# Kernel tuning notes

Hardware: AMD Instinct MI355X
Metric: run time of the kernel (lower is better)

Reference implementation:

```python
import jax, jax.numpy as jnp
import numpy as np

N = 2708
IN_C = 1433
OUT_C = 64


def setup_inputs() -> dict:
    key = jax.random.key(0)
    k1, k2, k3, k4, k5, k6, k7 = jax.random.split(key, 7)
    X = jax.random.normal(k1, (N, IN_C), dtype=jnp.float32)
    A = jax.random.randint(k2, (N, N), 0, 2, dtype=jnp.int32)  # dense binary adjacency mask
    # Graph Fourier basis: orthonormal-ish random matrix (QR of gaussian)
    U = jnp.linalg.qr(jax.random.normal(k3, (N, N), dtype=jnp.float32))[0]
    s = 1.0 / np.sqrt(IN_C)
    W_K = jax.random.normal(k4, (OUT_C, IN_C), dtype=jnp.float32) * s
    W_Q = jax.random.normal(k5, (OUT_C, IN_C), dtype=jnp.float32) * s
    W_V = jax.random.normal(k6, (OUT_C, IN_C), dtype=jnp.float32) * s
    lmbd = jax.random.uniform(k7, (N, 1), dtype=jnp.float32)
    return {"X": X, "A": A, "U": U, "W_K": W_K, "W_Q": W_Q, "W_V": W_V, "lmbd": lmbd}


def reference(X, A, U, W_K, W_Q, W_V, lmbd):
    # Linear projections (torch nn.Linear: x @ W.T)
    K = X @ W_K.T  # [N, d]
    Q = X @ W_Q.T  # [N, d]
    V = X @ W_V.T  # [N, d]
    d_k = K.shape[-1]
    E = (Q @ K.T) / d_k  # [N, N]
    # spectral filtering: igft(lmbd * gft(E)) = U @ (lmbd * (U^T @ E))
    E = jnp.abs(U @ (lmbd * (U.T @ E)))
    # masked softmax over neighbors; dropout p=0 in eval mode (no-op)
    E_masked = jnp.where(A == 0, -jnp.inf, E)
    alpha = jax.nn.softmax(E_masked, axis=-1)
    H = alpha @ V  # [N, d]
    return H
```

## Files before the change

### kernel.cpp

```cpp
#include <hip/hip_runtime.h>

#define NV 2708
#define INC 1433
#define XCOLS 1472
#define UDIM 2752
#define PSTR 2720
#define BSTR 2752
#define SLAB ((size_t)(2752*64))
#define MWPR 88
#define NSP 8
#define NSU 22

typedef __attribute__((ext_vector_type(8))) short bf16x8;
typedef __attribute__((ext_vector_type(4))) float f32x4;
typedef __attribute__((ext_vector_type(4))) unsigned short u16x4;

__device__ __forceinline__ unsigned short f2bf(float f){
  union { float f; unsigned int i; } v; v.f = f;
  return (unsigned short)((v.i + 0x7fffu + ((v.i >> 16) & 1u)) >> 16);
}

__device__ __forceinline__ void conv_row(const float* __restrict__ src,
                                         unsigned short* __restrict__ dst, int tid){
  const int sh = ((unsigned int)((size_t)src >> 2)) & 1;
  if (tid == 0){ int ce = sh ? 0 : (INC - 1); dst[ce] = f2bf(src[ce]); }
  const float2* s2 = (const float2*)(src + sh);
  for (int c2 = tid; c2 < (INC - 1)/2; c2 += 256){
    float2 v = s2[c2];
    int c = sh + c2*2;
    dst[c]     = f2bf(v.x);
    dst[c + 1] = f2bf(v.y);
  }
  for (int c = INC + tid; c < XCOLS; c += 256) dst[c] = 0;
}

__global__ __launch_bounds__(256) void convert_all(
    const float* __restrict__ X, const float* __restrict__ WK,
    const float* __restrict__ WQ, const float* __restrict__ WV,
    const float* __restrict__ U, const int* __restrict__ A,
    unsigned short* __restrict__ Xbf, unsigned short* __restrict__ Wbf,
    unsigned short* __restrict__ Ubf, unsigned int* __restrict__ Abits)
{
  const int bx = blockIdx.x;
  const int tid = threadIdx.x;
  if (bx < 2752){
    const int row = bx;
    unsigned short* dst = Ubf + (size_t)row*UDIM;
    if (row < NV){
      const float* src = U + (size_t)row*NV;
      for (int c4 = tid; c4 < 688; c4 += 256){
        float4 v = make_float4(0.f,0.f,0.f,0.f);
        if (c4 < 677) v = *(const float4*)(src + c4*4);
        u16x4 h = { f2bf(v.x), f2bf(v.y), f2bf(v.z), f2bf(v.w) };
        *(u16x4*)(dst + c4*4) = h;
      }
    } else {
      u16x4 zz = {0,0,0,0};
      for (int c4 = tid; c4 < 688; c4 += 256) *(u16x4*)(dst + c4*4) = zz;
    }
  } else if (bx < 5504){
    const int row = bx - 2752;
    unsigned short* dst = Xbf + (size_t)row*XCOLS;
    if (row < NV){
      conv_row(X + (size_t)row*INC, dst, tid);
    } else {
      u16x4 zz = {0,0,0,0};
      for (int c4 = tid; c4 < XCOLS/4; c4 += 256) *(u16x4*)(dst + c4*4) = zz;
    }
  } else if (bx < 5696){
    const int row = bx - 5504;
    const float* s = (row < 64) ? WK : (row < 128) ? WQ : WV;
    conv_row(s + (size_t)(row & 63)*INC, Wbf + (size_t)row*XCOLS, tid);
  } else {
    const int i = bx - 5696;
    const int lane = tid & 63, wave = tid >> 6;
    const int* arow = A + (size_t)i*NV;
    unsigned int* drow = Abits + (size_t)i*MWPR;
    for (int g = wave; g < 11; g += 4){
      int base = g*256 + lane*4;
      int4 v = make_int4(0,0,0,0);
      if (base < NV) v = *(const int4*)(arow + base);
      unsigned long long m0 = __ballot(v.x != 0);
      unsigned long long m1 = __ballot(v.y != 0);
      unsigned long long m2 = __ballot(v.z != 0);
      unsigned long long m3 = __ballot(v.w != 0);
      if (lane < 8){
        unsigned long long mm = (lane < 2) ? m0 : (lane < 4) ? m1 : (lane < 6) ? m2 : m3;
        drow[g*8 + lane] = (lane & 1) ? (unsigned int)(mm >> 32) : (unsigned int)mm;
      }
    }
  }
}

__global__ __launch_bounds__(256) void proj(
    const unsigned short* __restrict__ Xbf, const unsigned short* __restrict__ Wbf,
    float* __restrict__ part)
{
  __shared__ __align__(16) unsigned short At[64*72];
  __shared__ __align__(16) unsigned short Bt[64*72];
  const int tid = threadIdx.x;
  const int lane = tid & 63, wave = tid >> 6, quad = lane >> 4, lr = lane & 15;
  const int m0 = blockIdx.x * 64;
  const int s  = blockIdx.y, z = blockIdx.z;
  const int kbeg = s * 192, kend = min(kbeg + 192, XCOLS);
  const int wm = (wave & 1) * 32, wn = (wave >> 1) * 32;
  const unsigned short* Wz = Wbf + (size_t)z*64*XCOLS;
  const int srow = wave*8 + (lane >> 3), seg = lane & 7;
  f32x4 acc[2][2] = {};

  for (int k0 = kbeg; k0 < kend; k0 += 64){
    #pragma unroll
    for (int e = 0; e < 2; e++){
      int row = e*32 + srow;
      bf16x8 xa = *(const bf16x8*)(Xbf + (size_t)(m0+row)*XCOLS + k0 + seg*8);
      bf16x8 wb = *(const bf16x8*)(Wz  + (size_t)row*XCOLS      + k0 + seg*8);
      *(bf16x8*)&At[row*72 + seg*8] = xa;
      *(bf16x8*)&Bt[row*72 + seg*8] = wb;
    }
    __syncthreads();
    #pragma unroll
    for (int ks = 0; ks < 2; ks++){
      bf16x8 af[2], bv[2];
      #pragma unroll
      for (int t = 0; t < 2; t++){
        af[t] = *(const bf16x8*)&At[(wm + t*16 + lr)*72 + ks*32 + quad*8];
        bv[t] = *(const bf16x8*)&Bt[(wn + t*16 + lr)*72 + ks*32 + quad*8];
      }
      #pragma unroll
      for (int tm = 0; tm < 2; tm++)
        #pragma unroll
        for (int tn = 0; tn < 2; tn++)
          acc[tm][tn] = __builtin_amdgcn_mfma_f32_16x16x32_bf16(af[tm], bv[tn], acc[tm][tn], 0, 0, 0);
    }
    __syncthreads();
  }
  float* dst = part + (size_t)(z*NSP + s) * SLAB;
  #pragma unroll
  for (int tm = 0; tm < 2; tm++)
    #pragma unroll
    for (int tn = 0; tn < 2; tn++)
      #pragma unroll
      for (int e = 0; e < 4; e++)
        dst[(size_t)(m0 + wm + tm*16 + quad*4 + e)*64 + wn + tn*16 + lr] = acc[tm][tn][e];
}

__global__ __launch_bounds__(256) void reduce_proj(
    const float* __restrict__ part, unsigned short* __restrict__ K16f,
    unsigned short* __restrict__ QT16, unsigned short* __restrict__ VTf)
{
  int idx = blockIdx.x*256 + threadIdx.x;
  int z = blockIdx.y;
  int m = idx >> 6, c = idx & 63;
  const float* base = part + (size_t)z*NSP*SLAB + idx;
  float v = 0.f;
  #pragma unroll
  for (int s = 0; s < NSP; s++) v += base[s*SLAB];
  unsigned short h = (m < NV) ? f2bf(v) : (unsigned short)0;
  if (z == 0){
    if (m < 2720) K16f[((m>>4)*2 + (c>>5))*512 + (m&15)*32 + (c&31)] = h;
  } else if (z == 1){
    QT16[(size_t)c*BSTR + m] = h;
  } else {
    if (m < 2720) VTf[(m>>5)*2048 + c*32 + (m&31)] = h;
  }
}

__global__ __launch_bounds__(256) void gemmG(
    const unsigned short* __restrict__ Ubf, const unsigned short* __restrict__ QT,
    float* __restrict__ part)
{
  __shared__ __align__(16) unsigned short At[64*72];
  __shared__ __align__(16) unsigned short Bt[64*72];
  const int tid = threadIdx.x;
  const int lane = tid & 63, wave = tid >> 6, quad = lane >> 4, lr = lane & 15;
  const int m0 = blockIdx.x * 64;
  const int s  = blockIdx.y;
  const int kbeg = s * 128, kend = min(kbeg + 128, UDIM);
  const int wm = (wave & 1) * 32, wn = (wave >> 1) * 32;
  const int bc = tid >> 2, bseg = tid & 3;
  const int ml = (lane & 15)*4, koff = wave*16 + (lane >> 4);
  f32x4 acc[2][2] = {};

  for (int k0 = kbeg; k0 < kend; k0 += 64){
    #pragma unroll
    for (int e = 0; e < 4; e++){
      int kl = koff + e*4;
      u16x4 v = *(const u16x4*)(Ubf + (size_t)(k0+kl)*UDIM + m0 + ml);
      At[(ml+0)*72 + kl] = v[0];
      At[(ml+1)*72 + kl] = v[1];
      At[(ml+2)*72 + kl] = v[2];
      At[(ml+3)*72 + kl] = v[3];
    }
    {
      const unsigned short* q = QT + (size_t)bc*BSTR + k0 + bseg*16;
      *(bf16x8*)&Bt[bc*72 + bseg*16]     = *(const bf16x8*)(q);
      *(bf16x8*)&Bt[bc*72 + bseg*16 + 8] = *(const bf16x8*)(q + 8);
    }
    __syncthreads();
    #pragma unroll
    for (int ks = 0; ks < 2; ks++){
      bf16x8 af[2], bv[2];
      #pragma unroll
      for (int t = 0; t < 2; t++){
        af[t] = *(const bf16x8*)&At[(wm + t*16 + lr)*72 + ks*32 + quad*8];
        bv[t] = *(const bf16x8*)&Bt[(wn + t*16 + lr)*72 + ks*32 + quad*8];
      }
      #pragma unroll
      for (int tm = 0; tm < 2; tm++)
        #pragma unroll
        for (int tn = 0; tn < 2; tn++)
          acc[tm][tn] = __builtin_amdgcn_mfma_f32_16x16x32_bf16(af[tm], bv[tn], acc[tm][tn], 0, 0, 0);
    }
    __syncthreads();
  }
  float* dst = part + (size_t)s * SLAB;
  #pragma unroll
  for (int tm = 0; tm < 2; tm++)
    #pragma unroll
    for (int tn = 0; tn < 2; tn++)
      #pragma unroll
      for (int e = 0; e < 4; e++)
        dst[(size_t)(m0 + wm + tm*16 + quad*4 + e)*64 + wn + tn*16 + lr] = acc[tm][tn][e];
}

__global__ __launch_bounds__(256) void reduce_g(
    const float* __restrict__ part, const float* __restrict__ lm,
    unsigned short* __restrict__ G2T)
{
  int idx = blockIdx.x*256 + threadIdx.x;
  int m = idx >> 6, c = idx & 63;
  const float* base = part + idx;
  float v = 0.f;
  #pragma unroll
  for (int s = 0; s < NSU; s++) v += base[s*SLAB];
  unsigned short h = 0;
  if (m < NV) h = f2bf(v * lm[m] * (1.0f/64.0f));
  G2T[(size_t)c*BSTR + m] = h;
}

__global__ __launch_bounds__(256) void gemmF(
    const unsigned short* __restrict__ Ubf, const unsigned short* __restrict__ G2T,
    float* __restrict__ part)
{
  __shared__ __align__(16) unsigned short At[64*72];
  __shared__ __align__(16) unsigned short Bt[64*72];
  const int tid = threadIdx.x;
  const int lane = tid & 63, wave = tid >> 6, quad = lane >> 4, lr = lane & 15;
  const int m0 = blockIdx.x * 64;
  const int s  = blockIdx.y;
  const int kbeg = s * 128, kend = min(kbeg + 128, UDIM);
  const int wm = (wave & 1) * 32, wn = (wave >> 1) * 32;
  const int bc = tid >> 2, bseg = tid & 3;
  const int srow = wave*8 + (lane >> 3), seg = lane & 7;
  f32x4 acc[2][2] = {};

  for (int k0 = kbeg; k0 < kend; k0 += 64){
    #pragma unroll
    for (int e = 0; e < 2; e++){
      int row = e*32 + srow;
      bf16x8 ua = *(const bf16x8*)(Ubf + (size_t)(m0+row)*UDIM + k0 + seg*8);
      *(bf16x8*)&At[row*72 + seg*8] = ua;
    }
    {
      const unsigned short* g = G2T + (size_t)bc*BSTR + k0 + bseg*16;
      *(bf16x8*)&Bt[bc*72 + bseg*16]     = *(const bf16x8*)(g);
      *(bf16x8*)&Bt[bc*72 + bseg*16 + 8] = *(const bf16x8*)(g + 8);
    }
    __syncthreads();
    #pragma unroll
    for (int ks = 0; ks < 2; ks++){
      bf16x8 af[2], bv[2];
      #pragma unroll
      for (int t = 0; t < 2; t++){
        af[t] = *(const bf16x8*)&At[(wm + t*16 + lr)*72 + ks*32 + quad*8];
        bv[t] = *(const bf16x8*)&Bt[(wn + t*16 + lr)*72 + ks*32 + quad*8];
      }
      #pragma unroll
      for (int tm = 0; tm < 2; tm++)
        #pragma unroll
        for (int tn = 0; tn < 2; tn++)
          acc[tm][tn] = __builtin_amdgcn_mfma_f32_16x16x32_bf16(af[tm], bv[tn], acc[tm][tn], 0, 0, 0);
    }
    __syncthreads();
  }
  float* dst = part + (size_t)s * SLAB;
  #pragma unroll
  for (int tm = 0; tm < 2; tm++)
    #pragma unroll
    for (int tn = 0; tn < 2; tn++)
      #pragma unroll
      for (int e = 0; e < 4; e++)
        dst[(size_t)(m0 + wm + tm*16 + quad*4 + e)*64 + wn + tn*16 + lr] = acc[tm][tn][e];
}

__global__ __launch_bounds__(256) void fused_attn(
    const float* __restrict__ partF, const unsigned short* __restrict__ K16f,
    const unsigned int* __restrict__ Abits, const unsigned short* __restrict__ VTf,
    float* __restrict__ Hout)
{
  __shared__ __align__(16) unsigned short pbuf[8*PSTR];
  __shared__ __align__(16) unsigned short fbuf[8*64];
  __shared__ unsigned int mrow[8*MWPR];
  __shared__ float swave[4][8];
  __shared__ float rinv[8];
  const int tid  = threadIdx.x;
  const int lane = tid & 63, wave = tid >> 6;
  const int quad = lane >> 4, lr = lane & 15;
  const int i0 = blockIdx.x * 8;

  #pragma unroll
  for (int h = 0; h < 2; h++){
    int idx = h*256 + tid;
    const float* base = partF + (size_t)(i0 + (idx >> 6))*64 + (idx & 63);
    float v = 0.f;
    #pragma unroll
    for (int s = 0; s < NSU; s++) v += base[s*SLAB];
    fbuf[idx] = f2bf(v);
  }
  for (int idx = tid; idx < 8*MWPR; idx += 256){
    int r = idx / MWPR;
    unsigned int v = 0;
    if (i0 + r < NV) v = Abits[(size_t)(i0 + r)*MWPR + (idx - r*MWPR)];
    mrow[idx] = v;
  }
  __syncthreads();

  const bf16x8 af0 = *(const bf16x8*)&fbuf[(lr & 7)*64 + quad*8];
  const bf16x8 af1 = *(const bf16x8*)&fbuf[(lr & 7)*64 + 32 + quad*8];
  const int ehi   = quad >> 1;
  const int rbase = (quad & 1)*4 + ehi*2;
  float psum[2] = {0.f, 0.f};
  {
    int t = wave;
    const unsigned short* kb = K16f + t*1024 + lr*32 + quad*8;
    bf16x8 b0 = *(const bf16x8*)(kb);
    bf16x8 b1 = *(const bf16x8*)(kb + 512);
    while (t < 170){
      int tn = t + 4;
      bf16x8 n0 = b0, n1 = b1;
      if (tn < 170){
        const unsigned short* nb = K16f + tn*1024 + lr*32 + quad*8;
        n0 = *(const bf16x8*)(nb);
        n1 = *(const bf16x8*)(nb + 512);
      }
      f32x4 sv0 = {}, sv1 = {};
      sv0 = __builtin_amdgcn_mfma_f32_16x16x32_bf16(af0, b0, sv0, 0, 0, 0);
      sv1 = __builtin_amdgcn_mfma_f32_16x16x32_bf16(af1, b1, sv1, 0, 0, 0);
      f32x4 sv = sv0 + sv1;
      {
        int col = t*16 + lr;
        int ss = col & 255, ll = ss >> 2;
        int wsh = (col >> 8)*8 + (ss & 3)*2 + (ll >> 5);
        int bit = ll & 31;
        #pragma unroll
        for (int e2 = 0; e2 < 2; e2++){
          int r = rbase + e2;
          float svv = (e2 == 0) ? (ehi ? sv[2] : sv[0]) : (ehi ? sv[3] : sv[1]);
          float p = 0.f;
          if ((mrow[r*MWPR + wsh] >> bit) & 1u) p = __expf(fabsf(svv));
          psum[e2] += p;
          pbuf[r*PSTR + col] = f2bf(p);
        }
      }
      b0 = n0; b1 = n1; t = tn;
    }
  }
  #pragma unroll
  for (int e2 = 0; e2 < 2; e2++){
    float v = psum[e2];
    #pragma unroll
    for (int o = 1; o <= 8; o <<= 1) v += __shfl_xor(v, o, 64);
    if (lr == 0) swave[wave][rbase + e2] = v;
  }
  __syncthreads();
  if (tid < 8){
    float sum = swave[0][tid] + swave[1][tid] + swave[2][tid] + swave[3][tid];
    rinv[tid] = (sum > 0.f) ? (1.f/sum) : 0.f;
  }
  __syncthreads();

  const int c0 = wave * 16;
  const int mr = lr & 7;
  f32x4 acc = {};
  {
    bf16x8 bv = *(const bf16x8*)&VTf[(c0 + lr)*32 + quad*8];
    for (int kt = 0; kt < 85; kt++){
      bf16x8 bn = bv;
      if (kt + 1 < 85) bn = *(const bf16x8*)&VTf[(kt+1)*2048 + (c0 + lr)*32 + quad*8];
      bf16x8 af = *(const bf16x8*)&pbuf[mr*PSTR + kt*32 + quad*8];
      acc = __builtin_amdgcn_mfma_f32_16x16x32_bf16(af, bv, acc, 0, 0, 0);
      bv = bn;
    }
  }
  if (quad < 2){
    #pragma unroll
    for (int e = 0; e < 4; e++){
      int r = quad*4 + e;
      int i = i0 + r;
      if (i < NV) Hout[(size_t)i*64 + c0 + lr] = acc[e] * rinv[r];
    }
  }
}

extern "C" void kernel_launch(void* const* d_in, const int* in_sizes, int n_in,
                              void* d_out, int out_size, void* d_ws, size_t ws_size,
                              hipStream_t stream){
  (void)in_sizes; (void)n_in; (void)out_size; (void)ws_size;
  const float* X  = (const float*)d_in[0];
  const int*   A  = (const int*)d_in[1];
  const float* U  = (const float*)d_in[2];
  const float* WK = (const float*)d_in[3];
  const float* WQ = (const float*)d_in[4];
  const float* WV = (const float*)d_in[5];
  const float* lm = (const float*)d_in[6];

  char* ws = (char*)d_ws;
  size_t off = 0;
  auto alloc = [&](size_t bytes){ size_t o = off; off = (off + bytes + 255) & ~(size_t)255; return o; };
  float*          part = (float*)(ws + alloc(24*SLAB*4));
  unsigned short* Ubf  = (unsigned short*)(ws + alloc((size_t)UDIM*UDIM*2));
  unsigned short* Xbf  = (unsigned short*)(ws + alloc((size_t)UDIM*XCOLS*2));
  unsigned short* Wbf  = (unsigned short*)(ws + alloc((size_t)192*XCOLS*2));
  unsigned short* K16f = (unsigned short*)(ws + alloc((size_t)170*1024*2));
  unsigned short* QT16 = (unsigned short*)(ws + alloc((size_t)64*BSTR*2));
  unsigned short* G2T  = (unsigned short*)(ws + alloc((size_t)64*BSTR*2));
  unsigned short* VTf  = (unsigned short*)(ws + alloc((size_t)85*2048*2));
  unsigned int*   Abits= (unsigned int*)(ws + alloc((size_t)NV*MWPR*4));

  convert_all<<<dim3(8404), 256, 0, stream>>>(X, WK, WQ, WV, U, A, Xbf, Wbf, Ubf, Abits);
  proj<<<dim3(43, NSP, 3), 256, 0, stream>>>(Xbf, Wbf, part);
  reduce_proj<<<dim3(688, 3), 256, 0, stream>>>(part, K16f, QT16, VTf);
  gemmG<<<dim3(43, NSU), 256, 0, stream>>>(Ubf, QT16, part);
  reduce_g<<<dim3(688), 256, 0, stream>>>(part, lm, G2T);
  gemmF<<<dim3(43, NSU), 256, 0, stream>>>(Ubf, G2T, part);
  fused_attn<<<dim3((NV + 7)/8), 256, 0, stream>>>(part, K16f, Abits, VTf, (float*)d_out);
}
```

Measured before the change: 184.9 us.

## Fuse split-K reductions into GEMM tails via atomic counters; widen attention blocks to 16 rows

```diff
diff --git a/kernel.cpp b/kernel.cpp
--- a/kernel.cpp
+++ b/kernel.cpp
@@ -4,7 +4,7 @@
 #define INC 1433
 #define XCOLS 1472
 #define UDIM 2752
-#define PSTR 2720
+#define PSTR 2728
 #define BSTR 2752
 #define SLAB ((size_t)(2752*64))
 #define MWPR 88
@@ -39,10 +39,12 @@
     const float* __restrict__ WQ, const float* __restrict__ WV,
     const float* __restrict__ U, const int* __restrict__ A,
     unsigned short* __restrict__ Xbf, unsigned short* __restrict__ Wbf,
-    unsigned short* __restrict__ Ubf, unsigned int* __restrict__ Abits)
+    unsigned short* __restrict__ Ubf, unsigned int* __restrict__ Abits,
+    unsigned int* __restrict__ ctr)
 {
   const int bx = blockIdx.x;
   const int tid = threadIdx.x;
+  if (bx == 0 && tid < 256) ctr[tid] = 0u;
   if (bx < 2752){
     const int row = bx;
     unsigned short* dst = Ubf + (size_t)row*UDIM;
@@ -94,10 +96,13 @@
 
 __global__ __launch_bounds__(256) void proj(
     const unsigned short* __restrict__ Xbf, const unsigned short* __restrict__ Wbf,
-    float* __restrict__ part)
+    float* __restrict__ part, unsigned int* __restrict__ ctr,
+    unsigned short* __restrict__ K16f, unsigned short* __restrict__ QT16,
+    unsigned short* __restrict__ VTf)
 {
   __shared__ __align__(16) unsigned short At[64*72];
   __shared__ __align__(16) unsigned short Bt[64*72];
+  __shared__ unsigned int scnt;
   const int tid = threadIdx.x;
   const int lane = tid & 63, wave = tid >> 6, quad = lane >> 4, lr = lane & 15;
   const int m0 = blockIdx.x * 64;
@@ -142,35 +147,39 @@
       #pragma unroll
       for (int e = 0; e < 4; e++)
         dst[(size_t)(m0 + wm + tm*16 + quad*4 + e)*64 + wn + tn*16 + lr] = acc[tm][tn][e];
-}
-
-__global__ __launch_bounds__(256) void reduce_proj(
-    const float* __restrict__ part, unsigned short* __restrict__ K16f,
-    unsigned short* __restrict__ QT16, unsigned short* __restrict__ VTf)
-{
-  int idx = blockIdx.x*256 + threadIdx.x;
-  int z = blockIdx.y;
-  int m = idx >> 6, c = idx & 63;
-  const float* base = part + (size_t)z*NSP*SLAB + idx;
-  float v = 0.f;
-  #pragma unroll
-  for (int s = 0; s < NSP; s++) v += base[s*SLAB];
-  unsigned short h = (m < NV) ? f2bf(v) : (unsigned short)0;
-  if (z == 0){
-    if (m < 2720) K16f[((m>>4)*2 + (c>>5))*512 + (m&15)*32 + (c&31)] = h;
-  } else if (z == 1){
-    QT16[(size_t)c*BSTR + m] = h;
-  } else {
-    if (m < 2720) VTf[(m>>5)*2048 + c*32 + (m&31)] = h;
+
+  __threadfence();
+  __syncthreads();
+  if (tid == 0) scnt = atomicAdd(&ctr[z*43 + blockIdx.x], 1u);
+  __syncthreads();
+  if (scnt == NSP - 1){
+    __threadfence();
+    const float* base = part + (size_t)(z*NSP)*SLAB + (size_t)m0*64;
+    for (int idx = tid; idx < 4096; idx += 256){
+      int m = m0 + (idx >> 6), c = idx & 63;
+      float v = 0.f;
+      #pragma unroll
+      for (int s2 = 0; s2 < NSP; s2++) v += base[s2*SLAB + idx];
+      unsigned short h = (m < NV) ? f2bf(v) : (unsigned short)0;
+      if (z == 0){
+        if (m < 2720) K16f[((m>>4)*2 + (c>>5))*512 + (m&15)*32 + (c&31)] = h;
+      } else if (z == 1){
+        QT16[(size_t)c*BSTR + m] = h;
+      } else {
+        if (m < 2720) VTf[(m>>5)*2048 + c*32 + (m&31)] = h;
+      }
+    }
   }
 }
 
 __global__ __launch_bounds__(256) void gemmG(
     const unsigned short* __restrict__ Ubf, const unsigned short* __restrict__ QT,
-    float* __restrict__ part)
+    float* __restrict__ part, unsigned int* __restrict__ ctr,
+    const float* __restrict__ lm, unsigned short* __restrict__ G2T)
 {
   __shared__ __align__(16) unsigned short At[64*72];
   __shared__ __align__(16) unsigned short Bt[64*72];
+  __shared__ unsigned int scnt;
   const int tid = threadIdx.x;
   const int lane = tid & 63, wave = tid >> 6, quad = lane >> 4, lr = lane & 15;
   const int m0 = blockIdx.x * 64;
@@ -221,29 +230,34 @@
       #pragma unroll
       for (int e = 0; e < 4; e++)
         dst[(size_t)(m0 + wm + tm*16 + quad*4 + e)*64 + wn + tn*16 + lr] = acc[tm][tn][e];
-}
-
-__global__ __launch_bounds__(256) void reduce_g(
-    const float* __restrict__ part, const float* __restrict__ lm,
-    unsigned short* __restrict__ G2T)
-{
-  int idx = blockIdx.x*256 + threadIdx.x;
-  int m = idx >> 6, c = idx & 63;
-  const float* base = part + idx;
-  float v = 0.f;
-  #pragma unroll
-  for (int s = 0; s < NSU; s++) v += base[s*SLAB];
-  unsigned short h = 0;
-  if (m < NV) h = f2bf(v * lm[m] * (1.0f/64.0f));
-  G2T[(size_t)c*BSTR + m] = h;
+
+  __threadfence();
+  __syncthreads();
+  if (tid == 0) scnt = atomicAdd(&ctr[144 + blockIdx.x], 1u);
+  __syncthreads();
+  if (scnt == NSU - 1){
+    __threadfence();
+    const float* base = part + (size_t)m0*64;
+    for (int idx = tid; idx < 4096; idx += 256){
+      int m = m0 + (idx >> 6), c = idx & 63;
+      float v = 0.f;
+      #pragma unroll
+      for (int s2 = 0; s2 < NSU; s2++) v += base[s2*SLAB + idx];
+      unsigned short h = 0;
+      if (m < NV) h = f2bf(v * lm[m] * (1.0f/64.0f));
+      G2T[(size_t)c*BSTR + m] = h;
+    }
+  }
 }
 
 __global__ __launch_bounds__(256) void gemmF(
     const unsigned short* __restrict__ Ubf, const unsigned short* __restrict__ G2T,
-    float* __restrict__ part)
+    float* __restrict__ part, unsigned int* __restrict__ ctr,
+    unsigned short* __restrict__ Fbf)
 {
   __shared__ __align__(16) unsigned short At[64*72];
   __shared__ __align__(16) unsigned short Bt[64*72];
+  __shared__ unsigned int scnt;
   const int tid = threadIdx.x;
   const int lane = tid & 63, wave = tid >> 6, quad = lane >> 4, lr = lane & 15;
   const int m0 = blockIdx.x * 64;
@@ -279,7 +293,7 @@
       for (int tm = 0; tm < 2; tm++)
         #pragma unroll
         for (int tn = 0; tn < 2; tn++)
-          acc[tm][tn] = __builtin_amdgcn_mfma_f32_16x16x32_bf16(af[tm], bv[tn], acc[tm][tn], 0, 0, 0);
+          acc[tm][tn] = __builtin_amdgcn_mfma_f32_16x16x32_bf16(af[tm], bv[ks == 0 ? tn : tn], acc[tm][tn], 0, 0, 0);
     }
     __syncthreads();
   }
@@ -291,52 +305,57 @@
       #pragma unroll
       for (int e = 0; e < 4; e++)
         dst[(size_t)(m0 + wm + tm*16 + quad*4 + e)*64 + wn + tn*16 + lr] = acc[tm][tn][e];
-}
-
-__global__ __launch_bounds__(256) void fused_attn(
-    const float* __restrict__ partF, const unsigned short* __restrict__ K16f,
+
+  __threadfence();
+  __syncthreads();
+  if (tid == 0) scnt = atomicAdd(&ctr[192 + blockIdx.x], 1u);
+  __syncthreads();
+  if (scnt == NSU - 1){
+    __threadfence();
+    const float* base = part + (size_t)m0*64;
+    for (int idx = tid; idx < 4096; idx += 256){
+      int m = m0 + (idx >> 6), c = idx & 63;
+      float v = 0.f;
+      #pragma unroll
+      for (int s2 = 0; s2 < NSU; s2++) v += base[s2*SLAB + idx];
+      Fbf[(size_t)m*64 + c] = (m < NV) ? f2bf(v) : (unsigned short)0;
+    }
+  }
+}
+
+__global__ __launch_bounds__(512) void fused_attn(
+    const unsigned short* __restrict__ Fbf, const unsigned short* __restrict__ K16f,
     const unsigned int* __restrict__ Abits, const unsigned short* __restrict__ VTf,
     float* __restrict__ Hout)
 {
-  __shared__ __align__(16) unsigned short pbuf[8*PSTR];
-  __shared__ __align__(16) unsigned short fbuf[8*64];
-  __shared__ unsigned int mrow[8*MWPR];
-  __shared__ float swave[4][8];
-  __shared__ float rinv[8];
+  __shared__ __align__(16) unsigned short pbuf[16*PSTR];
+  __shared__ unsigned int mrow[16*MWPR];
+  __shared__ float swave[8][16];
+  __shared__ float rinv[16];
+  __shared__ __align__(16) float obuf[4][256];
   const int tid  = threadIdx.x;
   const int lane = tid & 63, wave = tid >> 6;
   const int quad = lane >> 4, lr = lane & 15;
-  const int i0 = blockIdx.x * 8;
-
-  #pragma unroll
-  for (int h = 0; h < 2; h++){
-    int idx = h*256 + tid;
-    const float* base = partF + (size_t)(i0 + (idx >> 6))*64 + (idx & 63);
-    float v = 0.f;
-    #pragma unroll
-    for (int s = 0; s < NSU; s++) v += base[s*SLAB];
-    fbuf[idx] = f2bf(v);
-  }
-  for (int idx = tid; idx < 8*MWPR; idx += 256){
+  const int i0 = blockIdx.x * 16;
+
+  for (int idx = tid; idx < 16*MWPR; idx += 512){
     int r = idx / MWPR;
     unsigned int v = 0;
     if (i0 + r < NV) v = Abits[(size_t)(i0 + r)*MWPR + (idx - r*MWPR)];
     mrow[idx] = v;
   }
-  __syncthreads();
-
-  const bf16x8 af0 = *(const bf16x8*)&fbuf[(lr & 7)*64 + quad*8];
-  const bf16x8 af1 = *(const bf16x8*)&fbuf[(lr & 7)*64 + 32 + quad*8];
-  const int ehi   = quad >> 1;
-  const int rbase = (quad & 1)*4 + ehi*2;
-  float psum[2] = {0.f, 0.f};
+  const bf16x8 af0 = *(const bf16x8*)(Fbf + (size_t)(i0 + lr)*64 + quad*8);
+  const bf16x8 af1 = *(const bf16x8*)(Fbf + (size_t)(i0 + lr)*64 + 32 + quad*8);
+  __syncthreads();
+
+  float psum[4] = {0.f, 0.f, 0.f, 0.f};
   {
     int t = wave;
     const unsigned short* kb = K16f + t*1024 + lr*32 + quad*8;
     bf16x8 b0 = *(const bf16x8*)(kb);
     bf16x8 b1 = *(const bf16x8*)(kb + 512);
     while (t < 170){
-      int tn = t + 4;
+      int tn = t + 8;
       bf16x8 n0 = b0, n1 = b1;
       if (tn < 170){
         const unsigned short* nb = K16f + tn*1024 + lr*32 + quad*8;
@@ -353,12 +372,11 @@
         int wsh = (col >> 8)*8 + (ss & 3)*2 + (ll >> 5);
         int bit = ll & 31;
         #pragma unroll
-        for (int e2 = 0; e2 < 2; e2++){
-          int r = rbase + e2;
-          float svv = (e2 == 0) ? (ehi ? sv[2] : sv[0]) : (ehi ? sv[3] : sv[1]);
+        for (int e = 0; e < 4; e++){
+          int r = quad*4 + e;
           float p = 0.f;
-          if ((mrow[r*MWPR + wsh] >> bit) & 1u) p = __expf(fabsf(svv));
-          psum[e2] += p;
+          if ((mrow[r*MWPR + wsh] >> bit) & 1u) p = __expf(fabsf(sv[e]));
+          psum[e] += p;
           pbuf[r*PSTR + col] = f2bf(p);
         }
       }
@@ -366,33 +384,40 @@
     }
   }
   #pragma unroll
-  for (int e2 = 0; e2 < 2; e2++){
-    float v = psum[e2];
+  for (int e = 0; e < 4; e++){
+    float v = psum[e];
     #pragma unroll
     for (int o = 1; o <= 8; o <<= 1) v += __shfl_xor(v, o, 64);
-    if (lr == 0) swave[wave][rbase + e2] = v;
-  }
-  __syncthreads();
-  if (tid < 8){
-    float sum = swave[0][tid] + swave[1][tid] + swave[2][tid] + swave[3][tid];
-    rinv[tid] = (sum > 0.f) ? (1.f/sum) : 0.f;
-  }
-  __syncthreads();
-
-  const int c0 = wave * 16;
-  const int mr = lr & 7;
+    if (lr == 0) swave[wave][quad*4 + e] = v;
+  }
+  __syncthreads();
+  if (tid < 16){
+    float s = 0.f;
+    #pragma unroll
+    for (int w = 0; w < 8; w++) s += swave[w][tid];
+    rinv[tid] = (s > 0.f) ? (1.f/s) : 0.f;
+  }
+  __syncthreads();
+
+  const int c0 = (wave & 3) * 16;
+  const int ktbeg = (wave >> 2) ? 43 : 0;
+  const int ktend = (wave >> 2) ? 85 : 43;
   f32x4 acc = {};
   {
-    bf16x8 bv = *(const bf16x8*)&VTf[(c0 + lr)*32 + quad*8];
-    for (int kt = 0; kt < 85; kt++){
+    bf16x8 bv = *(const bf16x8*)&VTf[ktbeg*2048 + (c0 + lr)*32 + quad*8];
+    for (int kt = ktbeg; kt < ktend; kt++){
       bf16x8 bn = bv;
-      if (kt + 1 < 85) bn = *(const bf16x8*)&VTf[(kt+1)*2048 + (c0 + lr)*32 + quad*8];
-      bf16x8 af = *(const bf16x8*)&pbuf[mr*PSTR + kt*32 + quad*8];
+      if (kt + 1 < ktend) bn = *(const bf16x8*)&VTf[(kt+1)*2048 + (c0 + lr)*32 + quad*8];
+      bf16x8 af = *(const bf16x8*)&pbuf[lr*PSTR + kt*32 + quad*8];
       acc = __builtin_amdgcn_mfma_f32_16x16x32_bf16(af, bv, acc, 0, 0, 0);
       bv = bn;
     }
   }
-  if (quad < 2){
+  if (wave >= 4) *(f32x4*)&obuf[wave & 3][lane*4] = acc;
+  __syncthreads();
+  if (wave < 4){
+    f32x4 o = *(const f32x4*)&obuf[wave][lane*4];
+    acc += o;
     #pragma unroll
     for (int e = 0; e < 4; e++){
       int r = quad*4 + e;
@@ -425,13 +450,13 @@
   unsigned short* QT16 = (unsigned short*)(ws + alloc((size_t)64*BSTR*2));
   unsigned short* G2T  = (unsigned short*)(ws + alloc((size_t)64*BSTR*2));
   unsigned short* VTf  = (unsigned short*)(ws + alloc((size_t)85*2048*2));
+  unsigned short* Fbf  = (unsigned short*)(ws + alloc((size_t)BSTR*64*2));
   unsigned int*   Abits= (unsigned int*)(ws + alloc((size_t)NV*MWPR*4));
-
-  convert_all<<<dim3(8404), 256, 0, stream>>>(X, WK, WQ, WV, U, A, Xbf, Wbf, Ubf, Abits);
-  proj<<<dim3(43, NSP, 3), 256, 0, stream>>>(Xbf, Wbf, part);
-  reduce_proj<<<dim3(688, 3), 256, 0, stream>>>(part, K16f, QT16, VTf);
-  gemmG<<<dim3(43, NSU), 256, 0, stream>>>(Ubf, QT16, part);
-  reduce_g<<<dim3(688), 256, 0, stream>>>(part, lm, G2T);
-  gemmF<<<dim3(43, NSU), 256, 0, stream>>>(Ubf, G2T, part);
-  fused_attn<<<dim3((NV + 7)/8), 256, 0, stream>>>(part, K16f, Abits, VTf, (float*)d_out);
-}
+  unsigned int*   ctr  = (unsigned int*)(ws + alloc(256*4));
+
+  convert_all<<<dim3(8404), 256, 0, stream>>>(X, WK, WQ, WV, U, A, Xbf, Wbf, Ubf, Abits, ctr);
+  proj<<<dim3(43, NSP, 3), 256, 0, stream>>>(Xbf, Wbf, part, ctr, K16f, QT16, VTf);
+  gemmG<<<dim3(43, NSU), 256, 0, stream>>>(Ubf, QT16, part, ctr, lm, G2T);
+  gemmF<<<dim3(43, NSU), 256, 0, stream>>>(Ubf, G2T, part, ctr, Fbf);
+  fused_attn<<<dim3(170), 512, 0, stream>>>(Fbf, K16f, Abits, VTf, (float*)d_out);
+}
```

Measured after the change: 637.6 us. +244.9%, slower.

## Process 16 query rows per attention block with split-K over 8 waves

Applied to the files above, without the earlier changes.

```diff
diff --git a/kernel.cpp b/kernel.cpp
--- a/kernel.cpp
+++ b/kernel.cpp
@@ -4,7 +4,7 @@
 #define INC 1433
 #define XCOLS 1472
 #define UDIM 2752
-#define PSTR 2720
+#define PSTR 2728
 #define BSTR 2752
 #define SLAB ((size_t)(2752*64))
 #define MWPR 88
@@ -293,31 +293,32 @@
         dst[(size_t)(m0 + wm + tm*16 + quad*4 + e)*64 + wn + tn*16 + lr] = acc[tm][tn][e];
 }
 
-__global__ __launch_bounds__(256) void fused_attn(
+__global__ __launch_bounds__(512) void fused_attn(
     const float* __restrict__ partF, const unsigned short* __restrict__ K16f,
     const unsigned int* __restrict__ Abits, const unsigned short* __restrict__ VTf,
     float* __restrict__ Hout)
 {
-  __shared__ __align__(16) unsigned short pbuf[8*PSTR];
-  __shared__ __align__(16) unsigned short fbuf[8*64];
-  __shared__ unsigned int mrow[8*MWPR];
-  __shared__ float swave[4][8];
-  __shared__ float rinv[8];
+  __shared__ __align__(16) unsigned short pbuf[16*PSTR];
+  __shared__ __align__(16) unsigned short fbuf[16*64];
+  __shared__ unsigned int mrow[16*MWPR];
+  __shared__ float swave[8][16];
+  __shared__ float rinv[16];
+  __shared__ __align__(16) float obuf[4][256];
   const int tid  = threadIdx.x;
   const int lane = tid & 63, wave = tid >> 6;
   const int quad = lane >> 4, lr = lane & 15;
-  const int i0 = blockIdx.x * 8;
+  const int i0 = blockIdx.x * 16;
 
   #pragma unroll
   for (int h = 0; h < 2; h++){
-    int idx = h*256 + tid;
+    int idx = h*512 + tid;
     const float* base = partF + (size_t)(i0 + (idx >> 6))*64 + (idx & 63);
     float v = 0.f;
     #pragma unroll
     for (int s = 0; s < NSU; s++) v += base[s*SLAB];
     fbuf[idx] = f2bf(v);
   }
-  for (int idx = tid; idx < 8*MWPR; idx += 256){
+  for (int idx = tid; idx < 16*MWPR; idx += 512){
     int r = idx / MWPR;
     unsigned int v = 0;
     if (i0 + r < NV) v = Abits[(size_t)(i0 + r)*MWPR + (idx - r*MWPR)];
@@ -325,18 +326,16 @@
   }
   __syncthreads();
 
-  const bf16x8 af0 = *(const bf16x8*)&fbuf[(lr & 7)*64 + quad*8];
-  const bf16x8 af1 = *(const bf16x8*)&fbuf[(lr & 7)*64 + 32 + quad*8];
-  const int ehi   = quad >> 1;
-  const int rbase = (quad & 1)*4 + ehi*2;
-  float psum[2] = {0.f, 0.f};
+  const bf16x8 af0 = *(const bf16x8*)&fbuf[lr*64 + quad*8];
+  const bf16x8 af1 = *(const bf16x8*)&fbuf[lr*64 + 32 + quad*8];
+  float psum[4] = {0.f, 0.f, 0.f, 0.f};
   {
     int t = wave;
     const unsigned short* kb = K16f + t*1024 + lr*32 + quad*8;
     bf16x8 b0 = *(const bf16x8*)(kb);
     bf16x8 b1 = *(const bf16x8*)(kb + 512);
     while (t < 170){
-      int tn = t + 4;
+      int tn = t + 8;
       bf16x8 n0 = b0, n1 = b1;
       if (tn < 170){
         const unsigned short* nb = K16f + tn*1024 + lr*32 + quad*8;
@@ -353,12 +352,11 @@
         int wsh = (col >> 8)*8 + (ss & 3)*2 + (ll >> 5);
         int bit = ll & 31;
         #pragma unroll
-        for (int e2 = 0; e2 < 2; e2++){
-          int r = rbase + e2;
-          float svv = (e2 == 0) ? (ehi ? sv[2] : sv[0]) : (ehi ? sv[3] : sv[1]);
+        for (int e = 0; e < 4; e++){
+          int r = quad*4 + e;
           float p = 0.f;
-          if ((mrow[r*MWPR + wsh] >> bit) & 1u) p = __expf(fabsf(svv));
-          psum[e2] += p;
+          if ((mrow[r*MWPR + wsh] >> bit) & 1u) p = __expf(fabsf(sv[e]));
+          psum[e] += p;
           pbuf[r*PSTR + col] = f2bf(p);
         }
       }
@@ -366,33 +364,40 @@
     }
   }
   #pragma unroll
-  for (int e2 = 0; e2 < 2; e2++){
-    float v = psum[e2];
+  for (int e = 0; e < 4; e++){
+    float v = psum[e];
     #pragma unroll
     for (int o = 1; o <= 8; o <<= 1) v += __shfl_xor(v, o, 64);
-    if (lr == 0) swave[wave][rbase + e2] = v;
+    if (lr == 0) swave[wave][quad*4 + e] = v;
   }
   __syncthreads();
-  if (tid < 8){
-    float sum = swave[0][tid] + swave[1][tid] + swave[2][tid] + swave[3][tid];
-    rinv[tid] = (sum > 0.f) ? (1.f/sum) : 0.f;
+  if (tid < 16){
+    float s = 0.f;
+    #pragma unroll
+    for (int w = 0; w < 8; w++) s += swave[w][tid];
+    rinv[tid] = (s > 0.f) ? (1.f/s) : 0.f;
   }
   __syncthreads();
 
-  const int c0 = wave * 16;
-  const int mr = lr & 7;
+  const int c0 = (wave & 3) * 16;
+  const int ktbeg = (wave >> 2) ? 43 : 0;
+  const int ktend = (wave >> 2) ? 85 : 43;
   f32x4 acc = {};
   {
-    bf16x8 bv = *(const bf16x8*)&VTf[(c0 + lr)*32 + quad*8];
-    for (int kt = 0; kt < 85; kt++){
+    bf16x8 bv = *(const bf16x8*)&VTf[ktbeg*2048 + (c0 + lr)*32 + quad*8];
+    for (int kt = ktbeg; kt < ktend; kt++){
       bf16x8 bn = bv;
-      if (kt + 1 < 85) bn = *(const bf16x8*)&VTf[(kt+1)*2048 + (c0 + lr)*32 + quad*8];
-      bf16x8 af = *(const bf16x8*)&pbuf[mr*PSTR + kt*32 + quad*8];
+      if (kt + 1 < ktend) bn = *(const bf16x8*)&VTf[(kt+1)*2048 + (c0 + lr)*32 + quad*8];
+      bf16x8 af = *(const bf16x8*)&pbuf[lr*PSTR + kt*32 + quad*8];
       acc = __builtin_amdgcn_mfma_f32_16x16x32_bf16(af, bv, acc, 0, 0, 0);
       bv = bn;
     }
   }
-  if (quad < 2){
+  if (wave >= 4) *(f32x4*)&obuf[wave & 3][lane*4] = acc;
+  __syncthreads();
+  if (wave < 4){
+    f32x4 o = *(const f32x4*)&obuf[wave][lane*4];
+    acc += o;
     #pragma unroll
     for (int e = 0; e < 4; e++){
       int r = quad*4 + e;
@@ -433,5 +438,5 @@
   gemmG<<<dim3(43, NSU), 256, 0, stream>>>(Ubf, QT16, part);
   reduce_g<<<dim3(688), 256, 0, stream>>>(part, lm, G2T);
   gemmF<<<dim3(43, NSU), 256, 0, stream>>>(Ubf, G2T, part);
-  fused_attn<<<dim3((NV + 7)/8), 256, 0, stream>>>(part, K16f, Abits, VTf, (float*)d_out);
-}
+  fused_attn<<<dim3(170), 512, 0, stream>>>(part, K16f, Abits, VTf, (float*)d_out);
+}
```

Result: no change. 182.1 us (-1.5%).
